# Optimization experiments

Measured on AMD Instinct MI355X. Metric: run time of the kernel, lower is better.

The kernel has to match this reference:

```python
import jax, jax.numpy as jnp
import numpy as np

B, T, D, H, DFF = 64, 100, 1024, 16, 4096
HD = D // H
EPS = 1e-5


def _rope_tables(t_len, hd, dtype):
    # matches RotaryEmbedding: inv_freq over even dims, emb = cat([freqs, freqs])
    inv_freq = 1.0 / (10000.0 ** (jnp.arange(0, hd, 2, dtype=jnp.float32) / hd))
    t = jnp.arange(t_len, dtype=jnp.float32)
    freqs = jnp.einsum('i,j->ij', t, inv_freq)          # (T, hd/2)
    emb = jnp.concatenate([freqs, freqs], axis=-1)      # (T, hd)
    # apply_rope uses cos[..., ::2] / sin[..., ::2]
    cos = jnp.cos(emb)[:, ::2].astype(dtype)            # (T, hd/2)
    sin = jnp.sin(emb)[:, ::2].astype(dtype)
    return cos, sin


def _apply_rope(x, cos, sin):
    # x: (B, H, T, hd); cos/sin: (T, hd/2) broadcast over B,H
    x1 = x[..., ::2]
    x2 = x[..., 1::2]
    return jnp.concatenate([x1 * cos - x2 * sin, x1 * sin + x2 * cos], axis=-1)


def _layernorm(x, g, b):
    mu = jnp.mean(x, axis=-1, keepdims=True)
    var = jnp.mean(jnp.square(x - mu), axis=-1, keepdims=True)
    return (x - mu) * jax.lax.rsqrt(var + EPS) * g + b


def setup_inputs() -> dict:
    key = jax.random.key(0)
    ks = jax.random.split(key, 8)
    s = 0.02
    return {
        'tgt': jax.random.normal(ks[0], (B, T, D), dtype=jnp.float32),
        'Wqkv': jax.random.normal(ks[1], (3 * D, D), dtype=jnp.float32) * s,
        'bqkv': jnp.zeros((3 * D,), jnp.float32),
        'Wo': jax.random.normal(ks[2], (D, D), dtype=jnp.float32) * s,
        'bo': jnp.zeros((D,), jnp.float32),
        'W1': jax.random.normal(ks[3], (DFF, D), dtype=jnp.float32) * s,
        'b1': jnp.zeros((DFF,), jnp.float32),
        'W2': jax.random.normal(ks[4], (D, DFF), dtype=jnp.float32) * s,
        'b2': jnp.zeros((D,), jnp.float32),
        'g1': jnp.ones((D,), jnp.float32),
        'be1': jnp.zeros((D,), jnp.float32),
        'g2': jnp.ones((D,), jnp.float32),
        'be2': jnp.zeros((D,), jnp.float32),
        'tgt_mask': jnp.tril(jnp.ones((T, T), jnp.int32)),
    }


def reference(tgt, Wqkv, bqkv, Wo, bo, W1, b1, W2, b2, g1, be1, g2, be2, tgt_mask):
    dtype = tgt.dtype
    # QKV projection (torch Linear: x @ W.T + b)
    qkv = jnp.einsum('btd,ed->bte', tgt, Wqkv) + bqkv          # (B,T,3D)
    qkv = qkv.reshape(B, T, 3, H, HD).transpose(2, 0, 3, 1, 4)  # (3,B,H,T,hd)
    q, k, v = qkv[0], qkv[1], qkv[2]

    cos, sin = _rope_tables(T, HD, dtype)
    q = _apply_rope(q, cos, sin)
    k = _apply_rope(k, cos, sin)

    scale = 1.0 / np.sqrt(HD)
    scores = jnp.einsum('bhqd,bhkd->bhqk', q, k) * scale        # (B,H,T,T)
    scores = jnp.where(tgt_mask == 0, -jnp.inf, scores)
    attn = jax.nn.softmax(scores, axis=-1)
    ctx = jnp.einsum('bhqk,bhkd->bhqd', attn, v)                # (B,H,T,hd)
    ctx = ctx.transpose(0, 2, 1, 3).reshape(B, T, D)

    tgt2 = jnp.einsum('btd,ed->bte', ctx, Wo) + bo
    x = _layernorm(tgt + tgt2, g1, be1)

    h = jax.nn.relu(jnp.einsum('btd,fd->btf', x, W1) + b1)
    ff = jnp.einsum('btf,df->btd', h, W2) + b2
    out = _layernorm(x + ff, g2, be2)
    return out
```

## Files before the change

kernel.cpp:

```cpp
#include <hip/hip_runtime.h>
#include <math.h>

#define Bn   64
#define Tn   100
#define Tp   128
#define Dn   1024
#define Hn   16
#define HDn  64
#define DFFn 4096
#define EPSf 1e-5f

typedef unsigned short ushort_t;
typedef __attribute__((ext_vector_type(8))) __bf16 bf16x8;
typedef __attribute__((ext_vector_type(4))) float f32x4;

__device__ __forceinline__ float u2f(ushort_t u) {
    union { unsigned int i; float f; } v; v.i = ((unsigned int)u) << 16; return v.f;
}
__device__ __forceinline__ ushort_t f2bf(float f) {
    union { float f; unsigned int u; } v; v.f = f;
    unsigned int r = v.u + 0x7FFFu + ((v.u >> 16) & 1u);
    return (ushort_t)(r >> 16);
}

__device__ __forceinline__ void gload_lds16(const void* g, void* l) {
    __builtin_amdgcn_global_load_lds(
        (const __attribute__((address_space(1))) unsigned int*)g,
        (__attribute__((address_space(3))) unsigned int*)l,
        16, 0, 0);
}

#define VMWAIT_(n) asm volatile("s_waitcnt vmcnt(" #n ")" ::: "memory")
#define VMWAIT(n)  VMWAIT_(n)

struct ConvSeg { const float* src; ushort_t* dst; int n4; };
struct Conv5   { ConvSeg seg[5]; float2* tab; };

__global__ __launch_bounds__(256) void conv_bf16_multi(Conv5 cfg)
{
    if (blockIdx.x == gridDim.x - 1) {
        for (int e = threadIdx.x; e < Tn * 16; e += 256) {
            const int t = e >> 4, f = e & 15;
            float s, c;
            sincosf((float)t * exp2f(-0.83048202f * (float)f), &s, &c);
            cfg.tab[e] = make_float2(c, s);
        }
        return;
    }
    int i = blockIdx.x * 256 + threadIdx.x;
    #pragma unroll
    for (int s = 0; s < 5; ++s) {
        const int n = cfg.seg[s].n4;
        if (i < n) {
            float4 v = ((const float4*)cfg.seg[s].src)[i];
            ushort4 o;
            o.x = f2bf(v.x); o.y = f2bf(v.y); o.z = f2bf(v.z); o.w = f2bf(v.w);
            ((ushort4*)cfg.seg[s].dst)[i] = o;
            return;
        }
        i -= n;
    }
}

#define GEMM_TILE_MAP(gx_, gy_, swz_)                                        \
    const int L  = blockIdx.x;                                               \
    int rowt, colt;                                                          \
    if (swz_) {                                                              \
        const int group = L / (8 * (gx_));                                   \
        int l = L - group * 8 * (gx_);                                       \
        const int rem = (gy_) - group * 8;                                   \
        if (rem >= 8) { rowt = group * 8 + (l & 7); colt = l >> 3; }         \
        else          { rowt = group * 8 + l % rem; colt = l / rem; }        \
    } else { rowt = L / (gx_); colt = L - rowt * (gx_); }

template<int BN, bool RELU, bool ADDRES, typename OutT>
__global__ __launch_bounds__(512, 2) void gemm256_bt(const ushort_t* __restrict__ A,
                                                     const ushort_t* __restrict__ Bm,
                                                     const float* __restrict__ bias,
                                                     const ushort_t* __restrict__ res,
                                                     OutT* __restrict__ C,
                                                     int M, int N, int K,
                                                     int gx, int swz)
{
    constexpr int JN = BN / 64;
    constexpr int NB = BN / 128;
    __shared__ __align__(16) ushort_t As[2][256 * 64];
    __shared__ __align__(16) ushort_t Bs[2][BN * 64];

    const int gy = M >> 8;
    GEMM_TILE_MAP(gx, gy, swz)

    const int tid  = threadIdx.x;
    const int lane = tid & 63;
    const int wave = tid >> 6;
    const int wm   = wave >> 2;
    const int wn   = wave & 3;
    const int row0 = rowt * 256;
    const int col0 = colt * BN;
    const int frow = lane & 15;
    const int g    = lane >> 4;

    auto stageA = [&](const ushort_t* src, int rowbase, ushort_t* lds) {
        #pragma unroll
        for (int i = 0; i < 2; ++i) {
            const int idx = i * 512 + tid;
            const int row = idx >> 3;
            const int gc  = (idx & 7) ^ (row & 7);
            gload_lds16(src + (size_t)(rowbase + row) * K + gc * 8, lds + idx * 8);
        }
    };
    auto stageB = [&](const ushort_t* src, int rowbase, ushort_t* lds) {
        #pragma unroll
        for (int i = 0; i < NB; ++i) {
            const int idx = i * 512 + tid;
            const int row = idx >> 3;
            const int gc  = (idx & 7) ^ (row & 7);
            gload_lds16(src + (size_t)(rowbase + row) * K + gc * 8, lds + idx * 8);
        }
    };

    f32x4 acc[8][JN] = {};

    const int NT = K >> 6;
    stageB(Bm,      col0,          &Bs[0][0]);
    stageB(Bm,      col0 + BN / 2, &Bs[0][(BN / 2) * 64]);
    stageA(A,       row0,          &As[0][0]);
    stageA(A,       row0 + 128,    &As[0][128 * 64]);
    stageB(Bm + 64, col0,          &Bs[1][0]);
    stageB(Bm + 64, col0 + BN / 2, &Bs[1][(BN / 2) * 64]);
    if constexpr (NB == 2) { VMWAIT(4); } else { VMWAIT(2); }
    __builtin_amdgcn_s_barrier();

    for (int t = 0; t < NT; ++t) {
        const int  buf = t & 1;
        const bool stA = (t + 1 < NT);
        const bool stB = (t + 2 < NT);

        if constexpr (BN == 128) {
            bf16x8 bfr[JN][2];
            #pragma unroll
            for (int j = 0; j < JN; ++j)
                #pragma unroll
                for (int kk = 0; kk < 2; ++kk) {
                    const int rb = wn * (BN / 4) + j * 16 + frow;
                    const int ch = kk * 4 + g;
                    bfr[j][kk] = *(const bf16x8*)&Bs[buf][rb * 64 + (ch ^ (rb & 7)) * 8];
                }
            bf16x8 af0[4][2];
            #pragma unroll
            for (int m = 0; m < 4; ++m)
                #pragma unroll
                for (int kk = 0; kk < 2; ++kk) {
                    const int ra = wm * 128 + m * 16 + frow;
                    const int ch = kk * 4 + g;
                    af0[m][kk] = *(const bf16x8*)&As[buf][ra * 64 + (ch ^ (ra & 7)) * 8];
                }
            if (stA) {
                stageA(A + (t + 1) * 64, row0,       &As[buf ^ 1][0]);
                stageA(A + (t + 1) * 64, row0 + 128, &As[buf ^ 1][128 * 64]);
            }
            __builtin_amdgcn_s_barrier();
            asm volatile("s_waitcnt lgkmcnt(0)" ::: "memory");
            __builtin_amdgcn_sched_barrier(0);
            __builtin_amdgcn_s_setprio(1);
            #pragma unroll
            for (int m = 0; m < 4; ++m)
                #pragma unroll
                for (int j = 0; j < JN; ++j)
                    #pragma unroll
                    for (int kk = 0; kk < 2; ++kk)
                        acc[m][j] = __builtin_amdgcn_mfma_f32_16x16x32_bf16(
                            af0[m][kk], bfr[j][kk], acc[m][j], 0, 0, 0);
            __builtin_amdgcn_s_setprio(0);
            __builtin_amdgcn_sched_barrier(0);
            __builtin_amdgcn_s_barrier();

            bf16x8 af1[4][2];
            #pragma unroll
            for (int m = 0; m < 4; ++m)
                #pragma unroll
                for (int kk = 0; kk < 2; ++kk) {
                    const int ra = wm * 128 + (4 + m) * 16 + frow;
                    const int ch = kk * 4 + g;
                    af1[m][kk] = *(const bf16x8*)&As[buf][ra * 64 + (ch ^ (ra & 7)) * 8];
                }
            if (stB) {
                stageB(Bm + (t + 2) * 64, col0,          &Bs[buf][0]);
                stageB(Bm + (t + 2) * 64, col0 + BN / 2, &Bs[buf][(BN / 2) * 64]);
            }
            __builtin_amdgcn_s_barrier();
            asm volatile("s_waitcnt lgkmcnt(0)" ::: "memory");
            __builtin_amdgcn_sched_barrier(0);
            __builtin_amdgcn_s_setprio(1);
            #pragma unroll
            for (int m = 0; m < 4; ++m)
                #pragma unroll
                for (int j = 0; j < JN; ++j)
                    #pragma unroll
                    for (int kk = 0; kk < 2; ++kk)
                        acc[4 + m][j] = __builtin_amdgcn_mfma_f32_16x16x32_bf16(
                            af1[m][kk], bfr[j][kk], acc[4 + m][j], 0, 0, 0);
            __builtin_amdgcn_s_setprio(0);
            __builtin_amdgcn_sched_barrier(0);
            if (stB)      { VMWAIT(2); }
            else if (stA) { VMWAIT(0); }
            __builtin_amdgcn_s_barrier();
        } else {
            bf16x8 bfr[JN][2];
            #pragma unroll
            for (int q = 0; q < 4; ++q) {
                bf16x8 af[2][2];
                #pragma unroll
                for (int ii = 0; ii < 2; ++ii)
                    #pragma unroll
                    for (int kk = 0; kk < 2; ++kk) {
                        const int ra = wm * 128 + (2 * q + ii) * 16 + frow;
                        const int ch = kk * 4 + g;
                        af[ii][kk] = *(const bf16x8*)&As[buf][ra * 64 + (ch ^ (ra & 7)) * 8];
                    }
                if (q == 0) {
                    #pragma unroll
                    for (int j = 0; j < JN; ++j)
                        #pragma unroll
                        for (int kk = 0; kk < 2; ++kk) {
                            const int rb = wn * (BN / 4) + j * 16 + frow;
                            const int ch = kk * 4 + g;
                            bfr[j][kk] = *(const bf16x8*)&Bs[buf][rb * 64 + (ch ^ (rb & 7)) * 8];
                        }
                }
                if (q == 0 && stA) stageA(A + (t + 1) * 64, row0,       &As[buf ^ 1][0]);
                if (q == 1 && stA) stageA(A + (t + 1) * 64, row0 + 128, &As[buf ^ 1][128 * 64]);
                if (q == 2 && stB) stageB(Bm + (t + 2) * 64, col0,          &Bs[buf][0]);
                if (q == 3 && stB) stageB(Bm + (t + 2) * 64, col0 + BN / 2, &Bs[buf][(BN / 2) * 64]);
                __builtin_amdgcn_s_barrier();
                asm volatile("s_waitcnt lgkmcnt(0)" ::: "memory");
                __builtin_amdgcn_sched_barrier(0);
                __builtin_amdgcn_s_setprio(1);
                #pragma unroll
                for (int ii = 0; ii < 2; ++ii)
                    #pragma unroll
                    for (int j = 0; j < JN; ++j)
                        #pragma unroll
                        for (int kk = 0; kk < 2; ++kk)
                            acc[2 * q + ii][j] = __builtin_amdgcn_mfma_f32_16x16x32_bf16(
                                af[ii][kk], bfr[j][kk], acc[2 * q + ii][j], 0, 0, 0);
                __builtin_amdgcn_s_setprio(0);
                __builtin_amdgcn_sched_barrier(0);
                if (q == 3) {
                    if (stB)      { VMWAIT(4); }
                    else if (stA) { VMWAIT(0); }
                }
                __builtin_amdgcn_s_barrier();
            }
        }
    }

    const int crow = (lane >> 4) * 4;
    const int ccol = lane & 15;
    #pragma unroll
    for (int i = 0; i < 8; ++i) {
        #pragma unroll
        for (int r = 0; r < 4; ++r) {
            const int row = row0 + wm * 128 + i * 16 + crow + r;
            #pragma unroll
            for (int j = 0; j < JN; ++j) {
                const int col = col0 + wn * (BN / 4) + j * 16 + ccol;
                float v = acc[i][j][r] + bias[col];
                if constexpr (ADDRES) v += u2f(res[(size_t)row * N + col]);
                if constexpr (RELU) v = fmaxf(v, 0.f);
                if constexpr (sizeof(OutT) == 2)
                    C[(size_t)row * N + col] = (OutT)f2bf(v);
                else
                    C[(size_t)row * N + col] = (OutT)v;
            }
        }
    }
}

__global__ __launch_bounds__(256) void rope_split(const ushort_t* __restrict__ qkv,
                                                  const float2*  __restrict__ tab,
                                                  ushort_t* __restrict__ q,
                                                  ushort_t* __restrict__ k,
                                                  ushort_t* __restrict__ vt)
{
    __shared__ ushort_t vls[64 * 130];

    const int bh  = blockIdx.x;
    const int b   = bh >> 4, h = bh & 15;
    const int tid = threadIdx.x;
    const size_t rowbase = (size_t)b * Tn * (3 * Dn) + h * HDn;

    const ushort_t* vsrc = qkv + rowbase + 2 * Dn;
    for (int idx = tid; idx < Tn * 64; idx += 256) {
        const int t = idx >> 6, d = idx & 63;
        vls[d * 130 + t] = vsrc[(size_t)t * (3 * Dn) + d];
    }

    #pragma unroll
    for (int s = 0; s < 2; ++s) {
        const ushort_t* src = qkv + rowbase + s * Dn;
        ushort_t* dst = (s ? k : q) + (size_t)bh * Tp * HDn;
        for (int idx = tid; idx < Tn * 32; idx += 256) {
            const int t = idx >> 5, p = idx & 31;
            const unsigned int xi =
                *(const unsigned int*)&src[(size_t)t * (3 * Dn) + 2 * p];
            const float x1 = u2f((ushort_t)(xi & 0xffffu));
            const float x2 = u2f((ushort_t)(xi >> 16));
            const float2 cs = tab[t * 16 + (p & 15)];
            dst[t * 64 + p]      = f2bf(x1 * cs.x - x2 * cs.y);
            dst[t * 64 + 32 + p] = f2bf(x1 * cs.y + x2 * cs.x);
        }
    }

    __syncthreads();

    ushort_t* vdst = vt + (size_t)bh * HDn * Tp;
    for (int idx = tid; idx < 64 * 64; idx += 256) {
        const int d  = idx >> 6;
        const int tt = (idx & 63) * 2;
        ushort2 o;
        o.x = (tt     < Tn) ? vls[d * 130 + tt]     : (ushort_t)0;
        o.y = (tt + 1 < Tn) ? vls[d * 130 + tt + 1] : (ushort_t)0;
        *(ushort2*)&vdst[d * Tp + tt] = o;
    }
}

__global__ __launch_bounds__(256) void attn_mfma(const ushort_t* __restrict__ q,
                                                 const ushort_t* __restrict__ k,
                                                 const ushort_t* __restrict__ vt,
                                                 ushort_t* __restrict__ ctx)
{
    __shared__ __align__(16) ushort_t sm[24576];

    const int bh   = blockIdx.x;
    const int b    = bh >> 4, h = bh & 15;
    const int tid  = threadIdx.x;
    const int wave = tid >> 6;
    const int lane = tid & 63;
    const int c    = lane & 15;
    const int g    = lane >> 4;
    const int R0   = wave * 32;

    const ushort_t* qg = q  + (size_t)bh * Tp * HDn;
    const ushort_t* kg = k  + (size_t)bh * Tp * HDn;
    const ushort_t* vg = vt + (size_t)bh * HDn * Tp;
    for (int s = wave; s < 16; s += 4) {
        const int idx = s * 64 + lane;
        { const int row = idx >> 3, pc = idx & 7, gc = pc ^ (row & 7);
          gload_lds16(qg + row * 64 + gc * 8, &sm[idx * 8]);
          gload_lds16(kg + row * 64 + gc * 8, &sm[8192 + idx * 8]); }
        { const int row = idx >> 4, pc = idx & 15, gc = pc ^ (row & 15);
          gload_lds16(vg + row * 128 + gc * 8, &sm[16384 + idx * 8]); }
    }
    __syncthreads();

    f32x4 acc[2][8] = {};
    #pragma unroll
    for (int ks = 0; ks < 2; ++ks) {
        const int cb = ks * 4;
        bf16x8 aq[2];
        #pragma unroll
        for (int i = 0; i < 2; ++i) {
            const int row = R0 + i * 16 + c;
            const int ph  = (cb + g) ^ (row & 7);
            aq[i] = *(const bf16x8*)&sm[row * 64 + ph * 8];
        }
        #pragma unroll
        for (int j = 0; j < 8; ++j) {
            const int row = j * 16 + c;
            const int ph  = (cb + g) ^ (row & 7);
            const bf16x8 bk = *(const bf16x8*)&sm[8192 + row * 64 + ph * 8];
            acc[0][j] = __builtin_amdgcn_mfma_f32_16x16x32_bf16(aq[0], bk, acc[0][j], 0, 0, 0);
            acc[1][j] = __builtin_amdgcn_mfma_f32_16x16x32_bf16(aq[1], bk, acc[1][j], 0, 0, 0);
        }
    }
    __syncthreads();

    float linv[2][4];
    #pragma unroll
    for (int i = 0; i < 2; ++i) {
        #pragma unroll
        for (int r = 0; r < 4; ++r) {
            const int row = R0 + i * 16 + g * 4 + r;
            float sv[8], m = -1e30f;
            #pragma unroll
            for (int j = 0; j < 8; ++j) {
                const int col = j * 16 + c;
                const float s = acc[i][j][r] * 0.125f;
                sv[j] = (col <= row) ? s : -1e30f;
                m = fmaxf(m, sv[j]);
            }
            #pragma unroll
            for (int msk = 1; msk < 16; msk <<= 1) m = fmaxf(m, __shfl_xor(m, msk));
            float l = 0.f;
            #pragma unroll
            for (int j = 0; j < 8; ++j) {
                const int col = j * 16 + c;
                const float p = (col <= row) ? __expf(sv[j] - m) : 0.f;
                sv[j] = p; l += p;
            }
            #pragma unroll
            for (int msk = 1; msk < 16; msk <<= 1) l += __shfl_xor(l, msk);
            linv[i][r] = 1.f / l;
            #pragma unroll
            for (int j = 0; j < 8; ++j) {
                const int chunk = j * 2 + (c >> 3);
                const int ph    = chunk ^ (row & 15);
                sm[row * 128 + ph * 8 + (c & 7)] = f2bf(sv[j]);
            }
        }
    }
    __syncthreads();

    f32x4 acc2[2][4] = {};
    #pragma unroll
    for (int ks = 0; ks < 4; ++ks) {
        const int cb = ks * 4;
        bf16x8 ap[2];
        #pragma unroll
        for (int i = 0; i < 2; ++i) {
            const int row = R0 + i * 16 + c;
            const int ph  = (cb + g) ^ (row & 15);
            ap[i] = *(const bf16x8*)&sm[row * 128 + ph * 8];
        }
        #pragma unroll
        for (int n = 0; n < 4; ++n) {
            const int row = n * 16 + c;
            const int ph  = (cb + g) ^ (row & 15);
            const bf16x8 bv = *(const bf16x8*)&sm[16384 + row * 128 + ph * 8];
            acc2[0][n] = __builtin_amdgcn_mfma_f32_16x16x32_bf16(ap[0], bv, acc2[0][n], 0, 0, 0);
            acc2[1][n] = __builtin_amdgcn_mfma_f32_16x16x32_bf16(ap[1], bv, acc2[1][n], 0, 0, 0);
        }
    }

    #pragma unroll
    for (int i = 0; i < 2; ++i) {
        #pragma unroll
        for (int r = 0; r < 4; ++r) {
            const int row = R0 + i * 16 + g * 4 + r;
            if (row < Tn) {
                const float s = linv[i][r];
                #pragma unroll
                for (int n = 0; n < 4; ++n) {
                    const int col = n * 16 + c;
                    ctx[(size_t)(b * Tn + row) * Dn + h * HDn + col] =
                        f2bf(acc2[i][n][r] * s);
                }
            }
        }
    }
}

__global__ __launch_bounds__(256) void ln_single(const ushort_t* __restrict__ a,
                                                 const float* __restrict__ g,
                                                 const float* __restrict__ be,
                                                 ushort_t* __restrict__ out_bf)
{
    const int row = blockIdx.x;
    const int tid = threadIdx.x;
    __shared__ float red[256];
    const size_t base = (size_t)row * Dn;

    float vals[4];
    float s = 0.f;
    #pragma unroll
    for (int i = 0; i < 4; ++i) {
        const int c = tid + i * 256;
        vals[i] = u2f(a[base + c]);
        s += vals[i];
    }
    red[tid] = s;
    __syncthreads();
    for (int o = 128; o > 0; o >>= 1) {
        if (tid < o) red[tid] += red[tid + o];
        __syncthreads();
    }
    const float mu = red[0] * (1.f / Dn);
    __syncthreads();

    float vs = 0.f;
    #pragma unroll
    for (int i = 0; i < 4; ++i) { const float d = vals[i] - mu; vs += d * d; }
    red[tid] = vs;
    __syncthreads();
    for (int o = 128; o > 0; o >>= 1) {
        if (tid < o) red[tid] += red[tid + o];
        __syncthreads();
    }
    const float rstd = rsqrtf(red[0] * (1.f / Dn) + EPSf);

    #pragma unroll
    for (int i = 0; i < 4; ++i) {
        const int c = tid + i * 256;
        out_bf[base + c] = f2bf((vals[i] - mu) * rstd * g[c] + be[c]);
    }
}

__global__ __launch_bounds__(256) void add_ln2(const ushort_t* __restrict__ a,
                                               const ushort_t* __restrict__ r,
                                               const float* __restrict__ g,
                                               const float* __restrict__ be,
                                               float* __restrict__ out)
{
    const int row = blockIdx.x;
    const int tid = threadIdx.x;
    __shared__ float red[256];
    const size_t base = (size_t)row * Dn;

    float vals[4];
    float s = 0.f;
    #pragma unroll
    for (int i = 0; i < 4; ++i) {
        const int c = tid + i * 256;
        vals[i] = u2f(a[base + c]) + u2f(r[base + c]);
        s += vals[i];
    }
    red[tid] = s;
    __syncthreads();
    for (int o = 128; o > 0; o >>= 1) {
        if (tid < o) red[tid] += red[tid + o];
        __syncthreads();
    }
    const float mu = red[0] * (1.f / Dn);
    __syncthreads();

    float vs = 0.f;
    #pragma unroll
    for (int i = 0; i < 4; ++i) { const float d = vals[i] - mu; vs += d * d; }
    red[tid] = vs;
    __syncthreads();
    for (int o = 128; o > 0; o >>= 1) {
        if (tid < o) red[tid] += red[tid + o];
        __syncthreads();
    }
    const float rstd = rsqrtf(red[0] * (1.f / Dn) + EPSf);

    #pragma unroll
    for (int i = 0; i < 4; ++i) {
        const int c = tid + i * 256;
        out[base + c] = (vals[i] - mu) * rstd * g[c] + be[c];
    }
}

extern "C" void kernel_launch(void* const* d_in, const int* in_sizes, int n_in,
                              void* d_out, int out_size, void* d_ws, size_t ws_size,
                              hipStream_t stream)
{
    const float* tgt  = (const float*)d_in[0];
    const float* Wqkv = (const float*)d_in[1];
    const float* bqkv = (const float*)d_in[2];
    const float* Wo   = (const float*)d_in[3];
    const float* bo   = (const float*)d_in[4];
    const float* W1   = (const float*)d_in[5];
    const float* b1   = (const float*)d_in[6];
    const float* W2   = (const float*)d_in[7];
    const float* b2   = (const float*)d_in[8];
    const float* g1   = (const float*)d_in[9];
    const float* be1  = (const float*)d_in[10];
    const float* g2   = (const float*)d_in[11];
    const float* be2  = (const float*)d_in[12];
    float* out = (float*)d_out;
    (void)in_sizes; (void)n_in; (void)out_size; (void)ws_size;

    const int M = Bn * Tn;

    char* w = (char*)d_ws;
    ushort_t* tgt_bf  = (ushort_t*)(w);
    ushort_t* Wqkv_bf = (ushort_t*)(w + 13107200);
    ushort_t* Wo_bf   = (ushort_t*)(w + 19398656);
    ushort_t* W1_bf   = (ushort_t*)(w + 21495808);
    ushort_t* W2_bf   = (ushort_t*)(w + 29884416);

    ushort_t* qb    = (ushort_t*)(w + 38273024);
    ushort_t* kb    = (ushort_t*)(w + 55050240);
    ushort_t* vtb   = (ushort_t*)(w + 71827456);
    ushort_t* hbuf  = (ushort_t*)(w + 38273024);
    ushort_t* qkvb  = (ushort_t*)(w + 88604672);
    ushort_t* ctxb  = (ushort_t*)(w + 88604672);
    ushort_t* tgt2b = (ushort_t*)(w + 101711872);
    ushort_t* ffb   = (ushort_t*)(w + 101711872);
    ushort_t* x_bf  = (ushort_t*)(w + 114819072);
    float2*   ropetab = (float2*)(w + 127926272);

    Conv5 cfg;
    cfg.seg[0] = { tgt,  tgt_bf,  M * Dn / 4 };
    cfg.seg[1] = { Wqkv, Wqkv_bf, 3 * Dn * Dn / 4 };
    cfg.seg[2] = { Wo,   Wo_bf,   Dn * Dn / 4 };
    cfg.seg[3] = { W1,   W1_bf,   DFFn * Dn / 4 };
    cfg.seg[4] = { W2,   W2_bf,   Dn * DFFn / 4 };
    cfg.tab    = ropetab;
    const int total4 = (M * Dn + 3 * Dn * Dn + Dn * Dn + 2 * DFFn * Dn) / 4;
    conv_bf16_multi<<<(total4 + 255) / 256 + 1, 256, 0, stream>>>(cfg);

    gemm256_bt<128, false, false, ushort_t><<<600, 512, 0, stream>>>(
        tgt_bf, Wqkv_bf, bqkv, nullptr, qkvb, M, 3 * Dn, Dn, 24, 1);
    rope_split<<<Bn * Hn, 256, 0, stream>>>(qkvb, ropetab, qb, kb, vtb);
    attn_mfma<<<Bn * Hn, 256, 0, stream>>>(qb, kb, vtb, ctxb);
    gemm256_bt<128, false, true, ushort_t><<<(Dn / 128) * (M / 256), 512, 0, stream>>>(
        ctxb, Wo_bf, bo, tgt_bf, tgt2b, M, Dn, Dn, Dn / 128, 1);
    ln_single<<<M, 256, 0, stream>>>(tgt2b, g1, be1, x_bf);
    gemm256_bt<256, true, false, ushort_t><<<(M / 256) * (DFFn / 256), 512, 0, stream>>>(
        x_bf, W1_bf, b1, nullptr, hbuf, M, DFFn, Dn, DFFn / 256, 0);
    gemm256_bt<128, false, false, ushort_t><<<(Dn / 128) * (M / 256), 512, 0, stream>>>(
        hbuf, W2_bf, b2, nullptr, ffb, M, Dn, DFFn, Dn / 128, 1);
    add_ln2<<<M, 256, 0, stream>>>(x_bf, ffb, g2, be2, out);
}
```

Before: 419.0 us.

## Use 128x128 double-buffered GEMM kernel for Wo and W2 projections

Adds a new 256-thread GEMM kernel with 128x128 tiles, swizzled LDS double buffering and staggered A/B prefetch, and uses it for the N=1024 output projection and FFN down-projection GEMMs. With M=6400 and N=1024 the old 256x128 tiling launched only 200 blocks. Smaller tiles double the block count and allow two blocks per CU, which should fill the GPU's CUs better. The cost is lower per-block data reuse, since each operand tile is reloaded more often overall.

```diff
diff --git a/kernel.cpp b/kernel.cpp
--- a/kernel.cpp
+++ b/kernel.cpp
@@ -277,6 +277,141 @@
     }
 }
 
+template<bool RELU, bool ADDRES, typename OutT>
+__global__ __launch_bounds__(256, 2) void gemm128_2p(const ushort_t* __restrict__ A,
+                                                     const ushort_t* __restrict__ Bm,
+                                                     const float* __restrict__ bias,
+                                                     const ushort_t* __restrict__ res,
+                                                     OutT* __restrict__ C,
+                                                     int M, int N, int K,
+                                                     int gx, int swz)
+{
+    __shared__ __align__(16) ushort_t As[2][128 * 64];
+    __shared__ __align__(16) ushort_t Bs[2][128 * 64];
+
+    const int gy = M >> 7;
+    GEMM_TILE_MAP(gx, gy, swz)
+
+    const int tid  = threadIdx.x;
+    const int lane = tid & 63;
+    const int wave = tid >> 6;
+    const int wrow = (wave >> 1) * 64;
+    const int wcol = (wave & 1) * 64;
+    const int row0 = rowt * 128;
+    const int col0 = colt * 128;
+    const int frow = lane & 15;
+    const int g    = lane >> 4;
+
+    auto stage = [&](const ushort_t* src, int rowbase, ushort_t* lds) {
+        #pragma unroll
+        for (int i = 0; i < 4; ++i) {
+            const int idx = i * 256 + tid;
+            const int row = idx >> 3;
+            const int gc  = (idx & 7) ^ (row & 7);
+            gload_lds16(src + (size_t)(rowbase + row) * K + gc * 8, lds + idx * 8);
+        }
+    };
+
+    f32x4 acc[4][4] = {};
+
+    const int NT = K >> 6;
+    stage(Bm,      col0, &Bs[0][0]);
+    stage(A,       row0, &As[0][0]);
+    stage(Bm + 64, col0, &Bs[1][0]);
+    VMWAIT(4);
+    __builtin_amdgcn_s_barrier();
+
+    for (int t = 0; t < NT; ++t) {
+        const int  buf = t & 1;
+        const bool stA = (t + 1 < NT);
+        const bool stB = (t + 2 < NT);
+
+        bf16x8 bfr[4][2];
+        #pragma unroll
+        for (int j = 0; j < 4; ++j)
+            #pragma unroll
+            for (int kk = 0; kk < 2; ++kk) {
+                const int rb = wcol + j * 16 + frow;
+                const int ch = kk * 4 + g;
+                bfr[j][kk] = *(const bf16x8*)&Bs[buf][rb * 64 + (ch ^ (rb & 7)) * 8];
+            }
+        bf16x8 af0[2][2];
+        #pragma unroll
+        for (int m = 0; m < 2; ++m)
+            #pragma unroll
+            for (int kk = 0; kk < 2; ++kk) {
+                const int ra = wrow + m * 16 + frow;
+                const int ch = kk * 4 + g;
+                af0[m][kk] = *(const bf16x8*)&As[buf][ra * 64 + (ch ^ (ra & 7)) * 8];
+            }
+        if (stA) stage(A + (t + 1) * 64, row0, &As[buf ^ 1][0]);
+        __builtin_amdgcn_s_barrier();
+        asm volatile("s_waitcnt lgkmcnt(0)" ::: "memory");
+        __builtin_amdgcn_sched_barrier(0);
+        __builtin_amdgcn_s_setprio(1);
+        #pragma unroll
+        for (int m = 0; m < 2; ++m)
+            #pragma unroll
+            for (int j = 0; j < 4; ++j)
+                #pragma unroll
+                for (int kk = 0; kk < 2; ++kk)
+                    acc[m][j] = __builtin_amdgcn_mfma_f32_16x16x32_bf16(
+                        af0[m][kk], bfr[j][kk], acc[m][j], 0, 0, 0);
+        __builtin_amdgcn_s_setprio(0);
+        __builtin_amdgcn_sched_barrier(0);
+        __builtin_amdgcn_s_barrier();
+
+        bf16x8 af1[2][2];
+        #pragma unroll
+        for (int m = 0; m < 2; ++m)
+            #pragma unroll
+            for (int kk = 0; kk < 2; ++kk) {
+                const int ra = wrow + (2 + m) * 16 + frow;
+                const int ch = kk * 4 + g;
+                af1[m][kk] = *(const bf16x8*)&As[buf][ra * 64 + (ch ^ (ra & 7)) * 8];
+            }
+        if (stB) stage(Bm + (t + 2) * 64, col0, &Bs[buf][0]);
+        __builtin_amdgcn_s_barrier();
+        asm volatile("s_waitcnt lgkmcnt(0)" ::: "memory");
+        __builtin_amdgcn_sched_barrier(0);
+        __builtin_amdgcn_s_setprio(1);
+        #pragma unroll
+        for (int m = 0; m < 2; ++m)
+            #pragma unroll
+            for (int j = 0; j < 4; ++j)
+                #pragma unroll
+                for (int kk = 0; kk < 2; ++kk)
+                    acc[2 + m][j] = __builtin_amdgcn_mfma_f32_16x16x32_bf16(
+                        af1[m][kk], bfr[j][kk], acc[2 + m][j], 0, 0, 0);
+        __builtin_amdgcn_s_setprio(0);
+        __builtin_amdgcn_sched_barrier(0);
+        if (stB)      { VMWAIT(4); }
+        else if (stA) { VMWAIT(0); }
+        __builtin_amdgcn_s_barrier();
+    }
+
+    const int crow = (lane >> 4) * 4;
+    const int ccol = lane & 15;
+    #pragma unroll
+    for (int i = 0; i < 4; ++i) {
+        #pragma unroll
+        for (int r = 0; r < 4; ++r) {
+            const int row = row0 + wrow + i * 16 + crow + r;
+            #pragma unroll
+            for (int j = 0; j < 4; ++j) {
+                const int col = col0 + wcol + j * 16 + ccol;
+                float v = acc[i][j][r] + bias[col];
+                if constexpr (ADDRES) v += u2f(res[(size_t)row * N + col]);
+                if constexpr (RELU) v = fmaxf(v, 0.f);
+                if constexpr (sizeof(OutT) == 2)
+                    C[(size_t)row * N + col] = (OutT)f2bf(v);
+                else
+                    C[(size_t)row * N + col] = (OutT)v;
+            }
+        }
+    }
+}
+
 __global__ __launch_bounds__(256) void rope_split(const ushort_t* __restrict__ qkv,
                                                   const float2*  __restrict__ tab,
                                                   ushort_t* __restrict__ q,
@@ -596,12 +731,12 @@
         tgt_bf, Wqkv_bf, bqkv, nullptr, qkvb, M, 3 * Dn, Dn, 24, 1);
     rope_split<<<Bn * Hn, 256, 0, stream>>>(qkvb, ropetab, qb, kb, vtb);
     attn_mfma<<<Bn * Hn, 256, 0, stream>>>(qb, kb, vtb, ctxb);
-    gemm256_bt<128, false, true, ushort_t><<<(Dn / 128) * (M / 256), 512, 0, stream>>>(
+    gemm128_2p<false, true, ushort_t><<<(M / 128) * (Dn / 128), 256, 0, stream>>>(
         ctxb, Wo_bf, bo, tgt_bf, tgt2b, M, Dn, Dn, Dn / 128, 1);
     ln_single<<<M, 256, 0, stream>>>(tgt2b, g1, be1, x_bf);
     gemm256_bt<256, true, false, ushort_t><<<(M / 256) * (DFFn / 256), 512, 0, stream>>>(
         x_bf, W1_bf, b1, nullptr, hbuf, M, DFFn, Dn, DFFn / 256, 0);
-    gemm256_bt<128, false, false, ushort_t><<<(Dn / 128) * (M / 256), 512, 0, stream>>>(
+    gemm128_2p<false, false, ushort_t><<<(M / 128) * (Dn / 128), 256, 0, stream>>>(
         hbuf, W2_bf, b2, nullptr, ffb, M, Dn, DFFn, Dn / 128, 1);
     add_ln2<<<M, 256, 0, stream>>>(x_bf, ffb, g2, be2, out);
 }
```

Result: faster. 399.3 us (-4.7%).

## Replace 256-row GEMM tiles with 128x128 tiles using 4-wave blocks

Applied to the files above, without the earlier changes.

Replaces the 512-thread GEMM with 256xBN tiles by a 256-thread kernel using 128x128 tiles, four waves each computing 64x64. The goal is more blocks for better CU fill and tail behaviour at M=6400, for example the QKV GEMM grows from 600 to 1200 blocks. The cost is less data reuse per tile, so more global and LDS traffic per flop, and fewer MFMAs between barriers.

```diff
diff --git a/kernel.cpp b/kernel.cpp
--- a/kernel.cpp
+++ b/kernel.cpp
@@ -73,8 +73,8 @@
         else          { rowt = group * 8 + l % rem; colt = l / rem; }        \
     } else { rowt = L / (gx_); colt = L - rowt * (gx_); }
 
-template<int BN, bool RELU, bool ADDRES, typename OutT>
-__global__ __launch_bounds__(512, 2) void gemm256_bt(const ushort_t* __restrict__ A,
+template<bool RELU, bool ADDRES, typename OutT>
+__global__ __launch_bounds__(256, 2) void gemm128_2p(const ushort_t* __restrict__ A,
                                                      const ushort_t* __restrict__ Bm,
                                                      const float* __restrict__ bias,
                                                      const ushort_t* __restrict__ res,
@@ -82,53 +82,39 @@
                                                      int M, int N, int K,
                                                      int gx, int swz)
 {
-    constexpr int JN = BN / 64;
-    constexpr int NB = BN / 128;
-    __shared__ __align__(16) ushort_t As[2][256 * 64];
-    __shared__ __align__(16) ushort_t Bs[2][BN * 64];
-
-    const int gy = M >> 8;
+    __shared__ __align__(16) ushort_t As[2][128 * 64];
+    __shared__ __align__(16) ushort_t Bs[2][128 * 64];
+
+    const int gy = M >> 7;
     GEMM_TILE_MAP(gx, gy, swz)
 
     const int tid  = threadIdx.x;
     const int lane = tid & 63;
     const int wave = tid >> 6;
-    const int wm   = wave >> 2;
-    const int wn   = wave & 3;
-    const int row0 = rowt * 256;
-    const int col0 = colt * BN;
+    const int wrow = (wave >> 1) * 64;
+    const int wcol = (wave & 1) * 64;
+    const int row0 = rowt * 128;
+    const int col0 = colt * 128;
     const int frow = lane & 15;
     const int g    = lane >> 4;
 
-    auto stageA = [&](const ushort_t* src, int rowbase, ushort_t* lds) {
-        #pragma unroll
-        for (int i = 0; i < 2; ++i) {
-            const int idx = i * 512 + tid;
+    auto stage = [&](const ushort_t* src, int rowbase, ushort_t* lds) {
+        #pragma unroll
+        for (int i = 0; i < 4; ++i) {
+            const int idx = i * 256 + tid;
             const int row = idx >> 3;
             const int gc  = (idx & 7) ^ (row & 7);
             gload_lds16(src + (size_t)(rowbase + row) * K + gc * 8, lds + idx * 8);
         }
     };
-    auto stageB = [&](const ushort_t* src, int rowbase, ushort_t* lds) {
-        #pragma unroll
-        for (int i = 0; i < NB; ++i) {
-            const int idx = i * 512 + tid;
-            const int row = idx >> 3;
-            const int gc  = (idx & 7) ^ (row & 7);
-            gload_lds16(src + (size_t)(rowbase + row) * K + gc * 8, lds + idx * 8);
-        }
-    };
-
-    f32x4 acc[8][JN] = {};
+
+    f32x4 acc[4][4] = {};
 
     const int NT = K >> 6;
-    stageB(Bm,      col0,          &Bs[0][0]);
-    stageB(Bm,      col0 + BN / 2, &Bs[0][(BN / 2) * 64]);
-    stageA(A,       row0,          &As[0][0]);
-    stageA(A,       row0 + 128,    &As[0][128 * 64]);
-    stageB(Bm + 64, col0,          &Bs[1][0]);
-    stageB(Bm + 64, col0 + BN / 2, &Bs[1][(BN / 2) * 64]);
-    if constexpr (NB == 2) { VMWAIT(4); } else { VMWAIT(2); }
+    stage(Bm,      col0, &Bs[0][0]);
+    stage(A,       row0, &As[0][0]);
+    stage(Bm + 64, col0, &Bs[1][0]);
+    VMWAIT(4);
     __builtin_amdgcn_s_barrier();
 
     for (int t = 0; t < NT; ++t) {
@@ -136,135 +122,80 @@
         const bool stA = (t + 1 < NT);
         const bool stB = (t + 2 < NT);
 
-        if constexpr (BN == 128) {
-            bf16x8 bfr[JN][2];
-            #pragma unroll
-            for (int j = 0; j < JN; ++j)
+        bf16x8 bfr[4][2];
+        #pragma unroll
+        for (int j = 0; j < 4; ++j)
+            #pragma unroll
+            for (int kk = 0; kk < 2; ++kk) {
+                const int rb = wcol + j * 16 + frow;
+                const int ch = kk * 4 + g;
+                bfr[j][kk] = *(const bf16x8*)&Bs[buf][rb * 64 + (ch ^ (rb & 7)) * 8];
+            }
+        bf16x8 af0[2][2];
+        #pragma unroll
+        for (int m = 0; m < 2; ++m)
+            #pragma unroll
+            for (int kk = 0; kk < 2; ++kk) {
+                const int ra = wrow + m * 16 + frow;
+                const int ch = kk * 4 + g;
+                af0[m][kk] = *(const bf16x8*)&As[buf][ra * 64 + (ch ^ (ra & 7)) * 8];
+            }
+        if (stA) stage(A + (t + 1) * 64, row0, &As[buf ^ 1][0]);
+        __builtin_amdgcn_s_barrier();
+        asm volatile("s_waitcnt lgkmcnt(0)" ::: "memory");
+        __builtin_amdgcn_sched_barrier(0);
+        __builtin_amdgcn_s_setprio(1);
+        #pragma unroll
+        for (int m = 0; m < 2; ++m)
+            #pragma unroll
+            for (int j = 0; j < 4; ++j)
                 #pragma unroll
-                for (int kk = 0; kk < 2; ++kk) {
-                    const int rb = wn * (BN / 4) + j * 16 + frow;
-                    const int ch = kk * 4 + g;
-                    bfr[j][kk] = *(const bf16x8*)&Bs[buf][rb * 64 + (ch ^ (rb & 7)) * 8];
-                }
-            bf16x8 af0[4][2];
-            #pragma unroll
-            for (int m = 0; m < 4; ++m)
+                for (int kk = 0; kk < 2; ++kk)
+                    acc[m][j] = __builtin_amdgcn_mfma_f32_16x16x32_bf16(
+                        af0[m][kk], bfr[j][kk], acc[m][j], 0, 0, 0);
+        __builtin_amdgcn_s_setprio(0);
+        __builtin_amdgcn_sched_barrier(0);
+        __builtin_amdgcn_s_barrier();
+
+        bf16x8 af1[2][2];
+        #pragma unroll
+        for (int m = 0; m < 2; ++m)
+            #pragma unroll
+            for (int kk = 0; kk < 2; ++kk) {
+                const int ra = wrow + (2 + m) * 16 + frow;
+                const int ch = kk * 4 + g;
+                af1[m][kk] = *(const bf16x8*)&As[buf][ra * 64 + (ch ^ (ra & 7)) * 8];
+            }
+        if (stB) stage(Bm + (t + 2) * 64, col0, &Bs[buf][0]);
+        __builtin_amdgcn_s_barrier();
+        asm volatile("s_waitcnt lgkmcnt(0)" ::: "memory");
+        __builtin_amdgcn_sched_barrier(0);
+        __builtin_amdgcn_s_setprio(1);
+        #pragma unroll
+        for (int m = 0; m < 2; ++m)
+            #pragma unroll
+            for (int j = 0; j < 4; ++j)
                 #pragma unroll
-                for (int kk = 0; kk < 2; ++kk) {
-                    const int ra = wm * 128 + m * 16 + frow;
-                    const int ch = kk * 4 + g;
-                    af0[m][kk] = *(const bf16x8*)&As[buf][ra * 64 + (ch ^ (ra & 7)) * 8];
-                }
-            if (stA) {
-                stageA(A + (t + 1) * 64, row0,       &As[buf ^ 1][0]);
-                stageA(A + (t + 1) * 64, row0 + 128, &As[buf ^ 1][128 * 64]);
-            }
-            __builtin_amdgcn_s_barrier();
-            asm volatile("s_waitcnt lgkmcnt(0)" ::: "memory");
-            __builtin_amdgcn_sched_barrier(0);
-            __builtin_amdgcn_s_setprio(1);
-            #pragma unroll
-            for (int m = 0; m < 4; ++m)
-                #pragma unroll
-                for (int j = 0; j < JN; ++j)
-                    #pragma unroll
-                    for (int kk = 0; kk < 2; ++kk)
-                        acc[m][j] = __builtin_amdgcn_mfma_f32_16x16x32_bf16(
-                            af0[m][kk], bfr[j][kk], acc[m][j], 0, 0, 0);
-            __builtin_amdgcn_s_setprio(0);
-            __builtin_amdgcn_sched_barrier(0);
-            __builtin_amdgcn_s_barrier();
-
-            bf16x8 af1[4][2];
-            #pragma unroll
-            for (int m = 0; m < 4; ++m)
-                #pragma unroll
-                for (int kk = 0; kk < 2; ++kk) {
-                    const int ra = wm * 128 + (4 + m) * 16 + frow;
-                    const int ch = kk * 4 + g;
-                    af1[m][kk] = *(const bf16x8*)&As[buf][ra * 64 + (ch ^ (ra & 7)) * 8];
-                }
-            if (stB) {
-                stageB(Bm + (t + 2) * 64, col0,          &Bs[buf][0]);
-                stageB(Bm + (t + 2) * 64, col0 + BN / 2, &Bs[buf][(BN / 2) * 64]);
-            }
-            __builtin_amdgcn_s_barrier();
-            asm volatile("s_waitcnt lgkmcnt(0)" ::: "memory");
-            __builtin_amdgcn_sched_barrier(0);
-            __builtin_amdgcn_s_setprio(1);
-            #pragma unroll
-            for (int m = 0; m < 4; ++m)
-                #pragma unroll
-                for (int j = 0; j < JN; ++j)
-                    #pragma unroll
-                    for (int kk = 0; kk < 2; ++kk)
-                        acc[4 + m][j] = __builtin_amdgcn_mfma_f32_16x16x32_bf16(
-                            af1[m][kk], bfr[j][kk], acc[4 + m][j], 0, 0, 0);
-            __builtin_amdgcn_s_setprio(0);
-            __builtin_amdgcn_sched_barrier(0);
-            if (stB)      { VMWAIT(2); }
-            else if (stA) { VMWAIT(0); }
-            __builtin_amdgcn_s_barrier();
-        } else {
-            bf16x8 bfr[JN][2];
-            #pragma unroll
-            for (int q = 0; q < 4; ++q) {
-                bf16x8 af[2][2];
-                #pragma unroll
-                for (int ii = 0; ii < 2; ++ii)
-                    #pragma unroll
-                    for (int kk = 0; kk < 2; ++kk) {
-                        const int ra = wm * 128 + (2 * q + ii) * 16 + frow;
-                        const int ch = kk * 4 + g;
-                        af[ii][kk] = *(const bf16x8*)&As[buf][ra * 64 + (ch ^ (ra & 7)) * 8];
-                    }
-                if (q == 0) {
-                    #pragma unroll
-                    for (int j = 0; j < JN; ++j)
-                        #pragma unroll
-                        for (int kk = 0; kk < 2; ++kk) {
-                            const int rb = wn * (BN / 4) + j * 16 + frow;
-                            const int ch = kk * 4 + g;
-                            bfr[j][kk] = *(const bf16x8*)&Bs[buf][rb * 64 + (ch ^ (rb & 7)) * 8];
-                        }
-                }
-                if (q == 0 && stA) stageA(A + (t + 1) * 64, row0,       &As[buf ^ 1][0]);
-                if (q == 1 && stA) stageA(A + (t + 1) * 64, row0 + 128, &As[buf ^ 1][128 * 64]);
-                if (q == 2 && stB) stageB(Bm + (t + 2) * 64, col0,          &Bs[buf][0]);
-                if (q == 3 && stB) stageB(Bm + (t + 2) * 64, col0 + BN / 2, &Bs[buf][(BN / 2) * 64]);
-                __builtin_amdgcn_s_barrier();
-                asm volatile("s_waitcnt lgkmcnt(0)" ::: "memory");
-                __builtin_amdgcn_sched_barrier(0);
-                __builtin_amdgcn_s_setprio(1);
-                #pragma unroll
-                for (int ii = 0; ii < 2; ++ii)
-                    #pragma unroll
-                    for (int j = 0; j < JN; ++j)
-                        #pragma unroll
-                        for (int kk = 0; kk < 2; ++kk)
-                            acc[2 * q + ii][j] = __builtin_amdgcn_mfma_f32_16x16x32_bf16(
-                                af[ii][kk], bfr[j][kk], acc[2 * q + ii][j], 0, 0, 0);
-                __builtin_amdgcn_s_setprio(0);
-                __builtin_amdgcn_sched_barrier(0);
-                if (q == 3) {
-                    if (stB)      { VMWAIT(4); }
-                    else if (stA) { VMWAIT(0); }
-                }
-                __builtin_amdgcn_s_barrier();
-            }
-        }
+                for (int kk = 0; kk < 2; ++kk)
+                    acc[2 + m][j] = __builtin_amdgcn_mfma_f32_16x16x32_bf16(
+                        af1[m][kk], bfr[j][kk], acc[2 + m][j], 0, 0, 0);
+        __builtin_amdgcn_s_setprio(0);
+        __builtin_amdgcn_sched_barrier(0);
+        if (stB)      { VMWAIT(4); }
+        else if (stA) { VMWAIT(0); }
+        __builtin_amdgcn_s_barrier();
     }
 
     const int crow = (lane >> 4) * 4;
     const int ccol = lane & 15;
     #pragma unroll
-    for (int i = 0; i < 8; ++i) {
+    for (int i = 0; i < 4; ++i) {
         #pragma unroll
         for (int r = 0; r < 4; ++r) {
-            const int row = row0 + wm * 128 + i * 16 + crow + r;
-            #pragma unroll
-            for (int j = 0; j < JN; ++j) {
-                const int col = col0 + wn * (BN / 4) + j * 16 + ccol;
+            const int row = row0 + wrow + i * 16 + crow + r;
+            #pragma unroll
+            for (int j = 0; j < 4; ++j) {
+                const int col = col0 + wcol + j * 16 + ccol;
                 float v = acc[i][j][r] + bias[col];
                 if constexpr (ADDRES) v += u2f(res[(size_t)row * N + col]);
                 if constexpr (RELU) v = fmaxf(v, 0.f);
@@ -592,16 +523,16 @@
     const int total4 = (M * Dn + 3 * Dn * Dn + Dn * Dn + 2 * DFFn * Dn) / 4;
     conv_bf16_multi<<<(total4 + 255) / 256 + 1, 256, 0, stream>>>(cfg);
 
-    gemm256_bt<128, false, false, ushort_t><<<600, 512, 0, stream>>>(
-        tgt_bf, Wqkv_bf, bqkv, nullptr, qkvb, M, 3 * Dn, Dn, 24, 1);
+    gemm128_2p<false, false, ushort_t><<<(M / 128) * (3 * Dn / 128), 256, 0, stream>>>(
+        tgt_bf, Wqkv_bf, bqkv, nullptr, qkvb, M, 3 * Dn, Dn, 3 * Dn / 128, 1);
     rope_split<<<Bn * Hn, 256, 0, stream>>>(qkvb, ropetab, qb, kb, vtb);
     attn_mfma<<<Bn * Hn, 256, 0, stream>>>(qb, kb, vtb, ctxb);
-    gemm256_bt<128, false, true, ushort_t><<<(Dn / 128) * (M / 256), 512, 0, stream>>>(
+    gemm128_2p<false, true, ushort_t><<<(M / 128) * (Dn / 128), 256, 0, stream>>>(
         ctxb, Wo_bf, bo, tgt_bf, tgt2b, M, Dn, Dn, Dn / 128, 1);
     ln_single<<<M, 256, 0, stream>>>(tgt2b, g1, be1, x_bf);
-    gemm256_bt<256, true, false, ushort_t><<<(M / 256) * (DFFn / 256), 512, 0, stream>>>(
-        x_bf, W1_bf, b1, nullptr, hbuf, M, DFFn, Dn, DFFn / 256, 0);
-    gemm256_bt<128, false, false, ushort_t><<<(Dn / 128) * (M / 256), 512, 0, stream>>>(
+    gemm128_2p<true, false, ushort_t><<<(M / 128) * (DFFn / 128), 256, 0, stream>>>(
+        x_bf, W1_bf, b1, nullptr, hbuf, M, DFFn, Dn, DFFn / 128, 0);
+    gemm128_2p<false, false, ushort_t><<<(M / 128) * (Dn / 128), 256, 0, stream>>>(
         hbuf, W2_bf, b2, nullptr, ffb, M, Dn, DFFn, Dn / 128, 1);
     add_ln2<<<M, 256, 0, stream>>>(x_bf, ffb, g2, be2, out);
 }
```

New measurement: 403.1 us. -3.8%, faster.
